# Kernel optimization log

Measured on AMD Instinct MI355X. Metric: run time of the kernel, lower is better.

## Reference

```python
import jax, jax.numpy as jnp
import numpy as np

N_NODES = 65536
N_EDGES = 1048576
D_IN = 1024
D_HID = 64
N_CLS = 32


def gcn_conv(x, W, b, src, dst, n_nodes):
    """PyG GCNConv: linear transform, then symmetric-normalized aggregation
    with implicit self-loops (fill value 1)."""
    xw = x @ W  # [N, d_out]
    e = src.shape[0]
    # degree over destination index, including the self-loop (+1)
    deg = jax.ops.segment_sum(jnp.ones((e,), xw.dtype), dst, num_segments=n_nodes) + 1.0
    dinv_sqrt = jax.lax.rsqrt(deg)  # deg >= 1, safe
    norm = dinv_sqrt[src] * dinv_sqrt[dst]  # [E]
    agg = jax.ops.segment_sum(xw[src] * norm[:, None], dst, num_segments=n_nodes)
    # self-loop contribution: norm = deg_i^{-1}
    agg = agg + xw * (1.0 / deg)[:, None]
    return agg + b


def setup_inputs() -> dict:
    key = jax.random.key(0)
    k_x, k_e, k_w1, k_b1, k_w2, k_b2 = jax.random.split(key, 6)
    x = jax.random.normal(k_x, (N_NODES, D_IN), dtype=jnp.float32)
    edge_index = jax.random.randint(k_e, (2, N_EDGES), 0, N_NODES, dtype=jnp.int64)
    s1 = 1.0 / np.sqrt(D_IN)
    s2 = 1.0 / np.sqrt(D_HID)
    W1 = jax.random.uniform(k_w1, (D_IN, D_HID), jnp.float32, -s1, s1)
    b1 = jax.random.uniform(k_b1, (D_HID,), jnp.float32, -s1, s1)
    W2 = jax.random.uniform(k_w2, (D_HID, N_CLS), jnp.float32, -s2, s2)
    b2 = jax.random.uniform(k_b2, (N_CLS,), jnp.float32, -s2, s2)
    return {"x": x, "edge_index": edge_index, "W1": W1, "b1": b1, "W2": W2, "b2": b2}


def reference(x, edge_index, W1, b1, W2, b2):
    src, dst = edge_index[0], edge_index[1]
    n = x.shape[0]
    h = gcn_conv(x, W1, b1, src, dst, n)
    h = jax.nn.relu(h)
    # dropout is identity in eval mode
    h = gcn_conv(h, W2, b2, src, dst, n)
    return jax.nn.log_softmax(h, axis=1)
```

## Files before the change

### kernel.cpp

```cpp
#include <hip/hip_runtime.h>
#include <hip/hip_bf16.h>

#define N_NODES 65536
#define D_IN 1024
#define D_HID 64
#define N_CLS 32

typedef short short8 __attribute__((ext_vector_type(8)));
typedef float floatx4 __attribute__((ext_vector_type(4)));

__global__ void k_count(const int* __restrict__ dst, int* __restrict__ cnt, int e4) {
  int i = blockIdx.x * blockDim.x + threadIdx.x;
  if (i < e4) {
    int4 d = ((const int4*)dst)[i];
    atomicAdd(&cnt[d.x], 1);
    atomicAdd(&cnt[d.y], 1);
    atomicAdd(&cnt[d.z], 1);
    atomicAdd(&cnt[d.w], 1);
  }
}

__global__ void k_dinv(const int* __restrict__ cnt, float* __restrict__ dinv) {
  int i = blockIdx.x * blockDim.x + threadIdx.x;
  if (i < N_NODES) dinv[i] = rsqrtf((float)(cnt[i] + 1));
}

__global__ void k_scan_a(const int* __restrict__ cnt, int* __restrict__ bsum) {
  __shared__ int s[256];
  int t = threadIdx.x;
  s[t] = cnt[blockIdx.x * 256 + t];
  __syncthreads();
  for (int off = 128; off > 0; off >>= 1) {
    if (t < off) s[t] += s[t + off];
    __syncthreads();
  }
  if (t == 0) bsum[blockIdx.x] = s[0];
}

__global__ void k_scan_b(int* __restrict__ bsum, int* __restrict__ boff) {
  __shared__ int s[256];
  int t = threadIdx.x;
  int v = bsum[t];
  s[t] = v;
  __syncthreads();
  for (int off = 1; off < 256; off <<= 1) {
    int x = (t >= off) ? s[t - off] : 0;
    __syncthreads();
    s[t] += x;
    __syncthreads();
  }
  boff[t] = s[t] - v;
}

__global__ void k_scan_c(const int* __restrict__ cnt, const int* __restrict__ boff,
                         int* __restrict__ rowptr, int* __restrict__ cursor) {
  __shared__ int s[256];
  int t = threadIdx.x;
  int i = blockIdx.x * 256 + t;
  int v = cnt[i];
  s[t] = v;
  __syncthreads();
  for (int off = 1; off < 256; off <<= 1) {
    int x = (t >= off) ? s[t - off] : 0;
    __syncthreads();
    s[t] += x;
    __syncthreads();
  }
  int excl = s[t] - v + boff[blockIdx.x];
  rowptr[i] = excl;
  cursor[i] = excl;
  if (i == N_NODES - 1) rowptr[N_NODES] = excl + v;
}

__global__ void k_fill(const int* __restrict__ src, const int* __restrict__ dst,
                       int* __restrict__ cursor, int* __restrict__ csr_src, int e4) {
  int i = blockIdx.x * blockDim.x + threadIdx.x;
  if (i < e4) {
    int4 d = ((const int4*)dst)[i];
    int4 s = ((const int4*)src)[i];
    csr_src[atomicAdd(&cursor[d.x], 1)] = s.x;
    csr_src[atomicAdd(&cursor[d.y], 1)] = s.y;
    csr_src[atomicAdd(&cursor[d.z], 1)] = s.z;
    csr_src[atomicAdd(&cursor[d.w], 1)] = s.w;
  }
}

__device__ __forceinline__ unsigned short f2bf(float f) {
  union { float f; unsigned u; } cv; cv.f = f;
  unsigned r = (cv.u + 0x7FFFu + ((cv.u >> 16) & 1u)) >> 16;
  return (unsigned short)r;
}

__global__ void k_w1t(const float* __restrict__ w1, unsigned short* __restrict__ w1t) {
  int i = blockIdx.x * blockDim.x + threadIdx.x;
  if (i < D_IN * D_HID) {
    int k = i / D_HID, n = i % D_HID;
    w1t[n * D_IN + k] = f2bf(w1[i]);
  }
}

__global__ __launch_bounds__(256) void k_gemm1(const float* __restrict__ x,
    const unsigned short* __restrict__ w1t, const float* __restrict__ dinv,
    float* __restrict__ xw1s) {
  int wave = threadIdx.x >> 6;
  int lane = threadIdx.x & 63;
  int quad = lane >> 4;
  int l16 = lane & 15;
  int rowbase = blockIdx.x * 64 + wave * 16;
  const float* xrow = x + (size_t)(rowbase + l16) * D_IN + quad * 8;
  floatx4 acc[4];
#pragma unroll
  for (int nt = 0; nt < 4; nt++) acc[nt] = (floatx4){0.f, 0.f, 0.f, 0.f};
  const unsigned short* bbase = w1t + quad * 8;
  for (int k0 = 0; k0 < D_IN; k0 += 32) {
    float4 a01 = *(const float4*)(xrow + k0);
    float4 a23 = *(const float4*)(xrow + k0 + 4);
    float av[8] = {a01.x, a01.y, a01.z, a01.w, a23.x, a23.y, a23.z, a23.w};
    short8 afrag;
#pragma unroll
    for (int j = 0; j < 8; j++) afrag[j] = (short)f2bf(av[j]);
#pragma unroll
    for (int nt = 0; nt < 4; nt++) {
      short8 bfrag = *(const short8*)(bbase + (size_t)(nt * 16 + l16) * D_IN + k0);
      acc[nt] = __builtin_amdgcn_mfma_f32_16x16x32_bf16(afrag, bfrag, acc[nt], 0, 0, 0);
    }
  }
#pragma unroll
  for (int r = 0; r < 4; r++) {
    int row = rowbase + quad * 4 + r;
    float sc = dinv[row];
#pragma unroll
    for (int nt = 0; nt < 4; nt++)
      xw1s[(size_t)row * D_HID + nt * 16 + l16] = acc[nt][r] * sc;
  }
}

__global__ __launch_bounds__(256) void k_agg1(const float* __restrict__ xw1s,
    const int* __restrict__ rowptr, const int* __restrict__ csr_src,
    const float* __restrict__ dinv, const float* __restrict__ b1,
    const float* __restrict__ w2, float* __restrict__ xw2s) {
  __shared__ float w2s[D_HID * N_CLS];
  __shared__ float hbuf[4][D_HID];
  for (int i = threadIdx.x; i < D_HID * N_CLS; i += 256) w2s[i] = w2[i];
  __syncthreads();
  int wave = threadIdx.x >> 6;
  int lane = threadIdx.x & 63;
  int node = blockIdx.x * 4 + wave;
  float dd = dinv[node];
  int beg = rowptr[node], end = rowptr[node + 1];
  float a0 = 0.f, a1 = 0.f, a2 = 0.f, a3 = 0.f;
  int e = beg;
  for (; e + 4 <= end; e += 4) {
    int s0 = csr_src[e], s1 = csr_src[e + 1], s2 = csr_src[e + 2], s3 = csr_src[e + 3];
    a0 += xw1s[(size_t)s0 * D_HID + lane];
    a1 += xw1s[(size_t)s1 * D_HID + lane];
    a2 += xw1s[(size_t)s2 * D_HID + lane];
    a3 += xw1s[(size_t)s3 * D_HID + lane];
  }
  for (; e < end; e++) a0 += xw1s[(size_t)csr_src[e] * D_HID + lane];
  float sum = (a0 + a1) + (a2 + a3);
  sum += xw1s[(size_t)node * D_HID + lane];
  float v = dd * sum + b1[lane];
  hbuf[wave][lane] = v > 0.f ? v : 0.f;
  __syncthreads();
  int half = lane >> 5, c = lane & 31;
  float p = 0.f;
#pragma unroll
  for (int kk = 0; kk < 32; kk++) {
    int k = half * 32 + kk;
    p += hbuf[wave][k] * w2s[k * N_CLS + c];
  }
  p += __shfl_down(p, 32);
  if (lane < 32) xw2s[(size_t)node * N_CLS + c] = p * dd;
}

__global__ __launch_bounds__(256) void k_agg2(const float* __restrict__ xw2s,
    const int* __restrict__ rowptr, const int* __restrict__ csr_src,
    const float* __restrict__ dinv, const float* __restrict__ b2,
    float* __restrict__ out) {
  int wave = threadIdx.x >> 6;
  int lane = threadIdx.x & 63;
  int node = blockIdx.x * 4 + wave;
  int half = lane >> 5, c = lane & 31;
  float dd = dinv[node];
  int beg = rowptr[node], end = rowptr[node + 1];
  float a0 = 0.f, a1 = 0.f;
  int e = beg + half;
  for (; e + 3 <= end; e += 4) {
    int s0 = csr_src[e], s1 = csr_src[e + 2];
    a0 += xw2s[(size_t)s0 * N_CLS + c];
    a1 += xw2s[(size_t)s1 * N_CLS + c];
  }
  for (; e < end; e += 2) a0 += xw2s[(size_t)csr_src[e] * N_CLS + c];
  float acc = a0 + a1;
  acc += __shfl_down(acc, 32);
  if (lane < 32) {
    acc += xw2s[(size_t)node * N_CLS + c];
    float logit = dd * acc + b2[c];
    float m = logit;
#pragma unroll
    for (int o = 16; o > 0; o >>= 1) m = fmaxf(m, __shfl_xor(m, o, 32));
    float ex = __expf(logit - m);
    float ssum = ex;
#pragma unroll
    for (int o = 16; o > 0; o >>= 1) ssum += __shfl_xor(ssum, o, 32);
    out[(size_t)node * N_CLS + c] = logit - m - __logf(ssum);
  }
}

extern "C" void kernel_launch(void* const* d_in, const int* in_sizes, int n_in,
                              void* d_out, int out_size, void* d_ws, size_t ws_size,
                              hipStream_t stream) {
  (void)n_in; (void)out_size; (void)ws_size;
  const float* x  = (const float*)d_in[0];
  const int*   ei = (const int*)d_in[1];
  const float* w1 = (const float*)d_in[2];
  const float* b1 = (const float*)d_in[3];
  const float* w2 = (const float*)d_in[4];
  const float* b2 = (const float*)d_in[5];
  float* out = (float*)d_out;
  int e = in_sizes[1] / 2;
  const int* src = ei;
  const int* dst = ei + e;

  char* ws = (char*)d_ws;
  int* cnt            = (int*)(ws + 0x000000);
  int* rowptr         = (int*)(ws + 0x040000);
  int* cursor         = (int*)(ws + 0x0C0000);
  float* dinv         = (float*)(ws + 0x100000);
  int* bsum           = (int*)(ws + 0x140000);
  int* boff           = (int*)(ws + 0x141000);
  int* csr_src        = (int*)(ws + 0x180000);
  unsigned short* w1t = (unsigned short*)(ws + 0x580000);
  float* xw1s         = (float*)(ws + 0x600000);
  float* xw2s         = (float*)(ws + 0x1600000);

  int e4 = e / 4;
  hipMemsetAsync(cnt, 0, N_NODES * sizeof(int), stream);
  k_count <<<(e4 + 255) / 256, 256, 0, stream>>>(dst, cnt, e4);
  k_dinv  <<<N_NODES / 256, 256, 0, stream>>>(cnt, dinv);
  k_scan_a<<<N_NODES / 256, 256, 0, stream>>>(cnt, bsum);
  k_scan_b<<<1, 256, 0, stream>>>(bsum, boff);
  k_scan_c<<<N_NODES / 256, 256, 0, stream>>>(cnt, boff, rowptr, cursor);
  k_fill  <<<(e4 + 255) / 256, 256, 0, stream>>>(src, dst, cursor, csr_src, e4);
  k_w1t   <<<(D_IN * D_HID) / 256, 256, 0, stream>>>(w1, w1t);
  k_gemm1 <<<N_NODES / 64, 256, 0, stream>>>(x, w1t, dinv, xw1s);
  k_agg1  <<<N_NODES / 4, 256, 0, stream>>>(xw1s, rowptr, csr_src, dinv, b1, w2, xw2s);
  k_agg2  <<<N_NODES / 4, 256, 0, stream>>>(xw2s, rowptr, csr_src, dinv, b2, out);
}
```

Baseline: 611.3 us.

## Store intermediates in bf16, fuse small kernels, widen GEMM tile and gather layout

Intermediate node features xw1s and xw2s are stored as bf16 instead of fp32, halving the bytes moved by the random gathers in both aggregation kernels. The dinv computation is folded into scan_c and the W1 transpose into the scan_b launch, removing two launches. The GEMM now computes two 16-row M tiles per wave so each B fragment is reused, and the aggregation kernels split edges across half-waves or quarter-waves using packed bf16 pairs. The cost is extra rounding error on the intermediates.

```diff
diff --git a/kernel.cpp b/kernel.cpp
--- a/kernel.cpp
+++ b/kernel.cpp
@@ -8,6 +8,21 @@
 
 typedef short short8 __attribute__((ext_vector_type(8)));
 typedef float floatx4 __attribute__((ext_vector_type(4)));
+
+__device__ __forceinline__ unsigned short f2bf(float f) {
+  union { float f; unsigned u; } cv; cv.f = f;
+  unsigned r = (cv.u + 0x7FFFu + ((cv.u >> 16) & 1u)) >> 16;
+  return (unsigned short)r;
+}
+__device__ __forceinline__ unsigned pack_bf2(float x, float y) {
+  return (unsigned)f2bf(x) | ((unsigned)f2bf(y) << 16);
+}
+__device__ __forceinline__ float2 bf2f2(unsigned v) {
+  union { unsigned u; float f; } a, b;
+  a.u = v << 16;
+  b.u = v & 0xFFFF0000u;
+  return make_float2(a.f, b.f);
+}
 
 __global__ void k_count(const int* __restrict__ dst, int* __restrict__ cnt, int e4) {
   int i = blockIdx.x * blockDim.x + threadIdx.x;
@@ -20,11 +35,6 @@
   }
 }
 
-__global__ void k_dinv(const int* __restrict__ cnt, float* __restrict__ dinv) {
-  int i = blockIdx.x * blockDim.x + threadIdx.x;
-  if (i < N_NODES) dinv[i] = rsqrtf((float)(cnt[i] + 1));
-}
-
 __global__ void k_scan_a(const int* __restrict__ cnt, int* __restrict__ bsum) {
   __shared__ int s[256];
   int t = threadIdx.x;
@@ -37,7 +47,14 @@
   if (t == 0) bsum[blockIdx.x] = s[0];
 }
 
-__global__ void k_scan_b(int* __restrict__ bsum, int* __restrict__ boff) {
+__global__ void k_scanb_w1t(int* __restrict__ bsum, int* __restrict__ boff,
+                            const float* __restrict__ w1, unsigned short* __restrict__ w1t) {
+  if (blockIdx.x < 256) {
+    int i = blockIdx.x * 256 + threadIdx.x;
+    int k = i / D_HID, n = i % D_HID;
+    w1t[n * D_IN + k] = f2bf(w1[i]);
+    return;
+  }
   __shared__ int s[256];
   int t = threadIdx.x;
   int v = bsum[t];
@@ -53,7 +70,8 @@
 }
 
 __global__ void k_scan_c(const int* __restrict__ cnt, const int* __restrict__ boff,
-                         int* __restrict__ rowptr, int* __restrict__ cursor) {
+                         int* __restrict__ rowptr, int* __restrict__ cursor,
+                         float* __restrict__ dinv) {
   __shared__ int s[256];
   int t = threadIdx.x;
   int i = blockIdx.x * 256 + t;
@@ -69,6 +87,7 @@
   int excl = s[t] - v + boff[blockIdx.x];
   rowptr[i] = excl;
   cursor[i] = excl;
+  dinv[i] = rsqrtf((float)(v + 1));
   if (i == N_NODES - 1) rowptr[N_NODES] = excl + v;
 }
 
@@ -85,126 +104,144 @@
   }
 }
 
-__device__ __forceinline__ unsigned short f2bf(float f) {
-  union { float f; unsigned u; } cv; cv.f = f;
-  unsigned r = (cv.u + 0x7FFFu + ((cv.u >> 16) & 1u)) >> 16;
-  return (unsigned short)r;
-}
-
-__global__ void k_w1t(const float* __restrict__ w1, unsigned short* __restrict__ w1t) {
-  int i = blockIdx.x * blockDim.x + threadIdx.x;
-  if (i < D_IN * D_HID) {
-    int k = i / D_HID, n = i % D_HID;
-    w1t[n * D_IN + k] = f2bf(w1[i]);
-  }
-}
-
 __global__ __launch_bounds__(256) void k_gemm1(const float* __restrict__ x,
     const unsigned short* __restrict__ w1t, const float* __restrict__ dinv,
-    float* __restrict__ xw1s) {
+    unsigned short* __restrict__ xw1s) {
   int wave = threadIdx.x >> 6;
   int lane = threadIdx.x & 63;
   int quad = lane >> 4;
   int l16 = lane & 15;
-  int rowbase = blockIdx.x * 64 + wave * 16;
-  const float* xrow = x + (size_t)(rowbase + l16) * D_IN + quad * 8;
-  floatx4 acc[4];
-#pragma unroll
-  for (int nt = 0; nt < 4; nt++) acc[nt] = (floatx4){0.f, 0.f, 0.f, 0.f};
+  int rowbase = blockIdx.x * 128 + wave * 32;
+  const float* xr0 = x + (size_t)(rowbase + l16) * D_IN + quad * 8;
+  const float* xr1 = xr0 + (size_t)16 * D_IN;
+  floatx4 acc[2][4];
+#pragma unroll
+  for (int mt = 0; mt < 2; mt++)
+#pragma unroll
+    for (int nt = 0; nt < 4; nt++) acc[mt][nt] = (floatx4){0.f, 0.f, 0.f, 0.f};
   const unsigned short* bbase = w1t + quad * 8;
+#pragma unroll 2
   for (int k0 = 0; k0 < D_IN; k0 += 32) {
-    float4 a01 = *(const float4*)(xrow + k0);
-    float4 a23 = *(const float4*)(xrow + k0 + 4);
-    float av[8] = {a01.x, a01.y, a01.z, a01.w, a23.x, a23.y, a23.z, a23.w};
-    short8 afrag;
-#pragma unroll
-    for (int j = 0; j < 8; j++) afrag[j] = (short)f2bf(av[j]);
+    float4 a0 = *(const float4*)(xr0 + k0);
+    float4 a1 = *(const float4*)(xr0 + k0 + 4);
+    float4 a2 = *(const float4*)(xr1 + k0);
+    float4 a3 = *(const float4*)(xr1 + k0 + 4);
+    float av0[8] = {a0.x, a0.y, a0.z, a0.w, a1.x, a1.y, a1.z, a1.w};
+    float av1[8] = {a2.x, a2.y, a2.z, a2.w, a3.x, a3.y, a3.z, a3.w};
+    short8 af0, af1;
+#pragma unroll
+    for (int j = 0; j < 8; j++) { af0[j] = (short)f2bf(av0[j]); af1[j] = (short)f2bf(av1[j]); }
 #pragma unroll
     for (int nt = 0; nt < 4; nt++) {
-      short8 bfrag = *(const short8*)(bbase + (size_t)(nt * 16 + l16) * D_IN + k0);
-      acc[nt] = __builtin_amdgcn_mfma_f32_16x16x32_bf16(afrag, bfrag, acc[nt], 0, 0, 0);
+      short8 bf = *(const short8*)(bbase + (size_t)(nt * 16 + l16) * D_IN + k0);
+      acc[0][nt] = __builtin_amdgcn_mfma_f32_16x16x32_bf16(af0, bf, acc[0][nt], 0, 0, 0);
+      acc[1][nt] = __builtin_amdgcn_mfma_f32_16x16x32_bf16(af1, bf, acc[1][nt], 0, 0, 0);
     }
   }
 #pragma unroll
-  for (int r = 0; r < 4; r++) {
-    int row = rowbase + quad * 4 + r;
-    float sc = dinv[row];
-#pragma unroll
-    for (int nt = 0; nt < 4; nt++)
-      xw1s[(size_t)row * D_HID + nt * 16 + l16] = acc[nt][r] * sc;
-  }
-}
-
-__global__ __launch_bounds__(256) void k_agg1(const float* __restrict__ xw1s,
+  for (int mt = 0; mt < 2; mt++)
+#pragma unroll
+    for (int r = 0; r < 4; r++) {
+      int row = rowbase + mt * 16 + quad * 4 + r;
+      float sc = dinv[row];
+#pragma unroll
+      for (int nt = 0; nt < 4; nt++)
+        xw1s[(size_t)row * D_HID + nt * 16 + l16] = f2bf(acc[mt][nt][r] * sc);
+    }
+}
+
+__global__ __launch_bounds__(256) void k_agg1(const unsigned* __restrict__ xw1s2,
     const int* __restrict__ rowptr, const int* __restrict__ csr_src,
     const float* __restrict__ dinv, const float* __restrict__ b1,
-    const float* __restrict__ w2, float* __restrict__ xw2s) {
+    const float* __restrict__ w2, unsigned short* __restrict__ xw2s) {
   __shared__ float w2s[D_HID * N_CLS];
-  __shared__ float hbuf[4][D_HID];
+  __shared__ float2 hbuf[4][32];
   for (int i = threadIdx.x; i < D_HID * N_CLS; i += 256) w2s[i] = w2[i];
   __syncthreads();
   int wave = threadIdx.x >> 6;
   int lane = threadIdx.x & 63;
+  int h = lane >> 5, l = lane & 31;
   int node = blockIdx.x * 4 + wave;
   float dd = dinv[node];
   int beg = rowptr[node], end = rowptr[node + 1];
-  float a0 = 0.f, a1 = 0.f, a2 = 0.f, a3 = 0.f;
-  int e = beg;
-  for (; e + 4 <= end; e += 4) {
-    int s0 = csr_src[e], s1 = csr_src[e + 1], s2 = csr_src[e + 2], s3 = csr_src[e + 3];
-    a0 += xw1s[(size_t)s0 * D_HID + lane];
-    a1 += xw1s[(size_t)s1 * D_HID + lane];
-    a2 += xw1s[(size_t)s2 * D_HID + lane];
-    a3 += xw1s[(size_t)s3 * D_HID + lane];
-  }
-  for (; e < end; e++) a0 += xw1s[(size_t)csr_src[e] * D_HID + lane];
-  float sum = (a0 + a1) + (a2 + a3);
-  sum += xw1s[(size_t)node * D_HID + lane];
-  float v = dd * sum + b1[lane];
-  hbuf[wave][lane] = v > 0.f ? v : 0.f;
-  __syncthreads();
-  int half = lane >> 5, c = lane & 31;
+  float2 c0 = {0.f, 0.f}, c1 = {0.f, 0.f}, c2 = {0.f, 0.f}, c3 = {0.f, 0.f};
+  int e = beg + h;
+  for (; e + 6 < end; e += 8) {
+    int s0 = csr_src[e], s1 = csr_src[e + 2], s2 = csr_src[e + 4], s3 = csr_src[e + 6];
+    float2 v0 = bf2f2(xw1s2[(size_t)s0 * 32 + l]);
+    float2 v1 = bf2f2(xw1s2[(size_t)s1 * 32 + l]);
+    float2 v2 = bf2f2(xw1s2[(size_t)s2 * 32 + l]);
+    float2 v3 = bf2f2(xw1s2[(size_t)s3 * 32 + l]);
+    c0.x += v0.x; c0.y += v0.y; c1.x += v1.x; c1.y += v1.y;
+    c2.x += v2.x; c2.y += v2.y; c3.x += v3.x; c3.y += v3.y;
+  }
+  for (; e < end; e += 2) {
+    float2 v = bf2f2(xw1s2[(size_t)csr_src[e] * 32 + l]);
+    c0.x += v.x; c0.y += v.y;
+  }
+  float sx = (c0.x + c1.x) + (c2.x + c3.x);
+  float sy = (c0.y + c1.y) + (c2.y + c3.y);
+  sx += __shfl_down(sx, 32);
+  sy += __shfl_down(sy, 32);
+  if (lane < 32) {
+    float2 self = bf2f2(xw1s2[(size_t)node * 32 + l]);
+    float2 bb = ((const float2*)b1)[l];
+    float vx = dd * (sx + self.x) + bb.x;
+    float vy = dd * (sy + self.y) + bb.y;
+    hbuf[wave][l] = make_float2(vx > 0.f ? vx : 0.f, vy > 0.f ? vy : 0.f);
+  }
+  __syncthreads();
+  const float* hb = (const float*)hbuf[wave];
+  int c = lane & 31;
   float p = 0.f;
 #pragma unroll
   for (int kk = 0; kk < 32; kk++) {
-    int k = half * 32 + kk;
-    p += hbuf[wave][k] * w2s[k * N_CLS + c];
+    int k = h * 32 + kk;
+    p += hb[k] * w2s[k * N_CLS + c];
   }
   p += __shfl_down(p, 32);
-  if (lane < 32) xw2s[(size_t)node * N_CLS + c] = p * dd;
-}
-
-__global__ __launch_bounds__(256) void k_agg2(const float* __restrict__ xw2s,
+  if (lane < 32) xw2s[(size_t)node * N_CLS + c] = f2bf(p * dd);
+}
+
+__global__ __launch_bounds__(256) void k_agg2(const unsigned* __restrict__ xw2s2,
     const int* __restrict__ rowptr, const int* __restrict__ csr_src,
     const float* __restrict__ dinv, const float* __restrict__ b2,
     float* __restrict__ out) {
   int wave = threadIdx.x >> 6;
   int lane = threadIdx.x & 63;
+  int q = lane >> 4, l = lane & 15;
   int node = blockIdx.x * 4 + wave;
-  int half = lane >> 5, c = lane & 31;
   float dd = dinv[node];
   int beg = rowptr[node], end = rowptr[node + 1];
-  float a0 = 0.f, a1 = 0.f;
-  int e = beg + half;
-  for (; e + 3 <= end; e += 4) {
-    int s0 = csr_src[e], s1 = csr_src[e + 2];
-    a0 += xw2s[(size_t)s0 * N_CLS + c];
-    a1 += xw2s[(size_t)s1 * N_CLS + c];
-  }
-  for (; e < end; e += 2) a0 += xw2s[(size_t)csr_src[e] * N_CLS + c];
-  float acc = a0 + a1;
-  acc += __shfl_down(acc, 32);
-  if (lane < 32) {
-    acc += xw2s[(size_t)node * N_CLS + c];
-    float logit = dd * acc + b2[c];
-    float m = logit;
-#pragma unroll
-    for (int o = 16; o > 0; o >>= 1) m = fmaxf(m, __shfl_xor(m, o, 32));
-    float ex = __expf(logit - m);
-    float ssum = ex;
-#pragma unroll
-    for (int o = 16; o > 0; o >>= 1) ssum += __shfl_xor(ssum, o, 32);
-    out[(size_t)node * N_CLS + c] = logit - m - __logf(ssum);
+  float2 c0 = {0.f, 0.f}, c1 = {0.f, 0.f};
+  int e = beg + q;
+  for (; e + 4 < end; e += 8) {
+    int s0 = csr_src[e], s1 = csr_src[e + 4];
+    float2 v0 = bf2f2(xw2s2[(size_t)s0 * 16 + l]);
+    float2 v1 = bf2f2(xw2s2[(size_t)s1 * 16 + l]);
+    c0.x += v0.x; c0.y += v0.y; c1.x += v1.x; c1.y += v1.y;
+  }
+  for (; e < end; e += 4) {
+    float2 v = bf2f2(xw2s2[(size_t)csr_src[e] * 16 + l]);
+    c0.x += v.x; c0.y += v.y;
+  }
+  float sx = c0.x + c1.x;
+  float sy = c0.y + c1.y;
+  sx += __shfl_down(sx, 32); sy += __shfl_down(sy, 32);
+  sx += __shfl_down(sx, 16); sy += __shfl_down(sy, 16);
+  if (lane < 16) {
+    float2 self = bf2f2(xw2s2[(size_t)node * 16 + l]);
+    float2 bb = ((const float2*)b2)[l];
+    float lx = dd * (sx + self.x) + bb.x;
+    float ly = dd * (sy + self.y) + bb.y;
+    float m = fmaxf(lx, ly);
+#pragma unroll
+    for (int o = 8; o > 0; o >>= 1) m = fmaxf(m, __shfl_xor(m, o));
+    float s2 = __expf(lx - m) + __expf(ly - m);
+#pragma unroll
+    for (int o = 8; o > 0; o >>= 1) s2 += __shfl_xor(s2, o);
+    float lse = m + __logf(s2);
+    ((float2*)out)[(size_t)node * 16 + l] = make_float2(lx - lse, ly - lse);
   }
 }
 
@@ -232,19 +269,19 @@
   int* boff           = (int*)(ws + 0x141000);
   int* csr_src        = (int*)(ws + 0x180000);
   unsigned short* w1t = (unsigned short*)(ws + 0x580000);
-  float* xw1s         = (float*)(ws + 0x600000);
-  float* xw2s         = (float*)(ws + 0x1600000);
+  unsigned short* xw1s= (unsigned short*)(ws + 0x600000);
+  unsigned short* xw2s= (unsigned short*)(ws + 0xE00000);
 
   int e4 = e / 4;
   hipMemsetAsync(cnt, 0, N_NODES * sizeof(int), stream);
-  k_count <<<(e4 + 255) / 256, 256, 0, stream>>>(dst, cnt, e4);
-  k_dinv  <<<N_NODES / 256, 256, 0, stream>>>(cnt, dinv);
-  k_scan_a<<<N_NODES / 256, 256, 0, stream>>>(cnt, bsum);
-  k_scan_b<<<1, 256, 0, stream>>>(bsum, boff);
-  k_scan_c<<<N_NODES / 256, 256, 0, stream>>>(cnt, boff, rowptr, cursor);
-  k_fill  <<<(e4 + 255) / 256, 256, 0, stream>>>(src, dst, cursor, csr_src, e4);
-  k_w1t   <<<(D_IN * D_HID) / 256, 256, 0, stream>>>(w1, w1t);
-  k_gemm1 <<<N_NODES / 64, 256, 0, stream>>>(x, w1t, dinv, xw1s);
-  k_agg1  <<<N_NODES / 4, 256, 0, stream>>>(xw1s, rowptr, csr_src, dinv, b1, w2, xw2s);
-  k_agg2  <<<N_NODES / 4, 256, 0, stream>>>(xw2s, rowptr, csr_src, dinv, b2, out);
-}
+  k_count   <<<(e4 + 255) / 256, 256, 0, stream>>>(dst, cnt, e4);
+  k_scan_a  <<<N_NODES / 256, 256, 0, stream>>>(cnt, bsum);
+  k_scanb_w1t<<<257, 256, 0, stream>>>(bsum, boff, w1, w1t);
+  k_scan_c  <<<N_NODES / 256, 256, 0, stream>>>(cnt, boff, rowptr, cursor, dinv);
+  k_fill    <<<(e4 + 255) / 256, 256, 0, stream>>>(src, dst, cursor, csr_src, e4);
+  k_gemm1   <<<N_NODES / 128, 256, 0, stream>>>(x, w1t, dinv, xw1s);
+  k_agg1    <<<N_NODES / 4, 256, 0, stream>>>((const unsigned*)xw1s, rowptr, csr_src,
+                                              dinv, b1, w2, xw2s);
+  k_agg2    <<<N_NODES / 4, 256, 0, stream>>>((const unsigned*)xw2s, rowptr, csr_src,
+                                              dinv, b2, out);
+}
```

Result: no change. 602.6 us (-1.4%).
